# Kernel tuning notes

Hardware: AMD Instinct MI355X
Metric: run time of the kernel (lower is better)

The kernel has to match this reference:

```python
import jax, jax.numpy as jnp
import numpy as np
import math

H = 8
C = 512
HIDE = 2048
LN_EPS = 1e-6


def setup_inputs() -> dict:
    key = jax.random.key(0)
    ks = jax.random.split(key, 9)
    B, N = 4, 2048
    std = 0.02
    return {
        "q": jax.random.normal(ks[0], (B, N, C), jnp.float32),
        "k": jax.random.normal(ks[1], (B, N, C), jnp.float32),
        "v": jax.random.normal(ks[2], (B, N, C), jnp.float32),
        "fc1_w": jax.random.normal(ks[3], (HIDE, C), jnp.float32) * std,
        "fc1_b": jnp.zeros((HIDE,), jnp.float32),
        "fc2_w": jax.random.normal(ks[4], (C, HIDE), jnp.float32) * std,
        "fc2_b": jnp.zeros((C,), jnp.float32),
        "ln1_w": jnp.ones((C,), jnp.float32),
        "ln1_b": jnp.zeros((C,), jnp.float32),
        "ln2_w": jnp.ones((C,), jnp.float32),
        "ln2_b": jnp.zeros((C,), jnp.float32),
    }


def _layernorm(x, w, b):
    mu = jnp.mean(x, axis=-1, keepdims=True)
    var = jnp.var(x, axis=-1, keepdims=True)
    return (x - mu) * jax.lax.rsqrt(var + LN_EPS) * w + b


def _mha(q, k, v):
    B, N, _ = q.shape
    hd = C // H
    # [B, H, N, hd]
    qh = q.reshape(B, N, H, hd).transpose(0, 2, 1, 3)
    kh = k.reshape(B, N, H, hd).transpose(0, 2, 1, 3)
    vh = v.reshape(B, N, H, hd).transpose(0, 2, 1, 3)
    scores = jnp.einsum('bhqd,bhkd->bhqk', qh, kh) / math.sqrt(hd)
    probs = jax.nn.softmax(scores, axis=-1)
    out = jnp.einsum('bhqk,bhkd->bhqd', probs, vh)
    return out.transpose(0, 2, 1, 3).reshape(B, N, C)


def reference(q, k, v, fc1_w, fc1_b, fc2_w, fc2_b, ln1_w, ln1_b, ln2_w, ln2_b):
    attn = _mha(q, k, v)
    q2 = _layernorm(q + attn, ln1_w, ln1_b)
    h = jax.nn.gelu(q2 @ fc1_w.T + fc1_b, approximate=False)
    mlp = h @ fc2_w.T + fc2_b
    return _layernorm(q2 + mlp, ln2_w, ln2_b)
```

## Files before the change

kernel.cpp:

```cpp
#include <hip/hip_runtime.h>
#include <math.h>

typedef unsigned short u16;
typedef __bf16 bf16_t;
typedef bf16_t bf16x4 __attribute__((ext_vector_type(4)));
typedef bf16_t bf16x8 __attribute__((ext_vector_type(8)));
typedef short s16x4 __attribute__((ext_vector_type(4)));
typedef float f32x4 __attribute__((ext_vector_type(4)));

typedef const __attribute__((address_space(1))) void* gcp;
typedef __attribute__((address_space(3))) void* lcp;

#define BB 4
#define NN 2048
#define CC 512
#define HH 8
#define HD 64
#define HIDE_ 2048
#define TT (BB*NN)

#if __has_builtin(__builtin_amdgcn_exp2f)
#define EXP2(x) __builtin_amdgcn_exp2f(x)
#else
#define EXP2(x) __expf((x) * 0.69314718055994531f)
#endif

#if __has_builtin(__builtin_amdgcn_rcpf)
#define RCP(x) __builtin_amdgcn_rcpf(x)
#else
#define RCP(x) (1.0f / (x))
#endif

__device__ __forceinline__ u16 f2bf(float f) {
  unsigned u = __float_as_uint(f);
  u += 0x7FFF + ((u >> 16) & 1);
  return (u16)(u >> 16);
}

__device__ __forceinline__ void bf8_to_f(const u16* p, float* f) {
  uint4 u = *(const uint4*)p;
  f[0] = __uint_as_float(u.x << 16); f[1] = __uint_as_float(u.x & 0xffff0000u);
  f[2] = __uint_as_float(u.y << 16); f[3] = __uint_as_float(u.y & 0xffff0000u);
  f[4] = __uint_as_float(u.z << 16); f[5] = __uint_as_float(u.z & 0xffff0000u);
  f[6] = __uint_as_float(u.w << 16); f[7] = __uint_as_float(u.w & 0xffff0000u);
}

__device__ __forceinline__ float gelu_tanh(float x) {
  float y = 0.7978845608028654f * x * (1.0f + 0.044715f * x * x);
  float a = y * 2.8853900817779268f;
  a = fminf(fmaxf(a, -30.0f), 30.0f);
  float e = EXP2(a);
  float t = (e - 1.0f) * RCP(e + 1.0f);
  return 0.5f * x * (1.0f + t);
}

__global__ __launch_bounds__(256) void prep_kernel(const float* __restrict__ q,
                                                   const float* __restrict__ k,
                                                   const float* __restrict__ fc1w,
                                                   const float* __restrict__ fc2w,
                                                   const float* __restrict__ v,
                                                   u16* __restrict__ qb,
                                                   u16* __restrict__ kb,
                                                   u16* __restrict__ w1b,
                                                   u16* __restrict__ w2b,
                                                   u16* __restrict__ vtb,
                                                   float qscale) {
  __shared__ __align__(16) u16 T[64 * 72];
  int bid = blockIdx.x, tid = threadIdx.x;
  if (bid < 5120) {
    const float* in;
    u16* out;
    int rel;
    float sc = 1.0f;
    if (bid < 2048)      { in = q;    out = qb;  rel = bid;        sc = qscale; }
    else if (bid < 4096) { in = k;    out = kb;  rel = bid - 2048; }
    else if (bid < 4608) { in = fc1w; out = w1b; rel = bid - 4096; }
    else                 { in = fc2w; out = w2b; rel = bid - 4608; }
    int i = (rel * 256 + tid) * 8;
    float4 a = *(const float4*)(in + i);
    float4 b2 = *(const float4*)(in + i + 4);
    u16 r[8] = {f2bf(a.x * sc), f2bf(a.y * sc), f2bf(a.z * sc), f2bf(a.w * sc),
                f2bf(b2.x * sc), f2bf(b2.y * sc), f2bf(b2.z * sc), f2bf(b2.w * sc)};
    *(uint4*)(out + i) = *(const uint4*)r;
    return;
  }
  int tv = bid - 5120;
  int j0 = (tv & 31) * 64;
  int bh = tv >> 5;
  int b = bh >> 3, h = bh & 7;
#pragma unroll
  for (int i = 0; i < 16; i++) {
    int idx = i * 256 + tid;
    int j = idx >> 6, d = idx & 63;
    T[d * 72 + j] = f2bf(v[((size_t)(b * NN + j0 + j)) * CC + h * 64 + d]);
  }
  __syncthreads();
#pragma unroll
  for (int i = 0; i < 16; i++) {
    int idx = i * 256 + tid;
    int d = idx >> 6, j = idx & 63;
    vtb[((size_t)(bh * 64 + d)) * NN + j0 + j] = T[d * 72 + j];
  }
}

__global__ __launch_bounds__(256, 8) void attn_kernel(const u16* __restrict__ qb,
                                                      const u16* __restrict__ kb,
                                                      const u16* __restrict__ vtb,
                                                      float* __restrict__ ou,
                                                      float* __restrict__ lsum) {
  __shared__ __align__(16) u16 Ks[64 * 64];
  __shared__ __align__(16) u16 Vs[64 * 64];
  int tid = threadIdx.x, wave = tid >> 6, lane = tid & 63;
  int l15 = lane & 15, quad = lane >> 4;
  int r7 = l15 & 7;
  int bid = blockIdx.x;
  int half = blockIdx.y;
  int qt = bid & 31, h = (bid >> 5) & 7, b = bid >> 8;
  int qw = qt * 64 + wave * 16;
  int j0base = half * 1024;

  float* ou_ = ou + (size_t)half * TT * CC;
  float* ls_ = lsum + (size_t)half * TT * HH;

  size_t qbase = ((size_t)(b * NN + qw + l15)) * CC + h * 64 + quad * 8;
  bf16x8 qf0 = *(const bf16x8*)&qb[qbase];
  bf16x8 qf1 = *(const bf16x8*)&qb[qbase + 32];

  int rl = lane >> 3;
  int cb = (lane & 7) ^ rl;
  int rK = wave * 16 + rl;
  size_t vtbase = ((size_t)(b * HH + h)) * 64 * NN;
  const u16* kp0 = kb + ((size_t)(b * NN + j0base + rK)) * CC + h * 64 + cb * 8;
  const u16* kp1 = kp0 + (size_t)8 * CC;
  const u16* vp0 = vtb + vtbase + (size_t)rK * NN + j0base + cb * 8;
  const u16* vp1 = vp0 + (size_t)8 * NN;
  lcp lK0 = (lcp)&Ks[wave * 16 * 64];
  lcp lK1 = (lcp)&Ks[wave * 16 * 64 + 8 * 64];
  lcp lV0 = (lcp)&Vs[wave * 16 * 64];
  lcp lV1 = (lcp)&Vs[wave * 16 * 64 + 8 * 64];

  float l_p = 0.f;
  f32x4 o[4] = {};

  for (int kt = 0; kt < 16; kt++) {
    __syncthreads();
    __builtin_amdgcn_global_load_lds((gcp)kp0, lK0, 16, 0, 0);
    __builtin_amdgcn_global_load_lds((gcp)kp1, lK1, 16, 0, 0);
    __builtin_amdgcn_global_load_lds((gcp)vp0, lV0, 16, 0, 0);
    __builtin_amdgcn_global_load_lds((gcp)vp1, lV1, 16, 0, 0);
    kp0 += (size_t)64 * CC; kp1 += (size_t)64 * CC;
    vp0 += 64; vp1 += 64;
    __syncthreads();

    s16x4 pf[4];
#pragma unroll
    for (int nt = 0; nt < 4; nt++) {
      f32x4 z = {0.f, 0.f, 0.f, 0.f};
      const u16* krow = &Ks[(nt * 16 + l15) * 64];
      bf16x8 k0 = *(const bf16x8*)&krow[(quad ^ r7) * 8];
      bf16x8 k1 = *(const bf16x8*)&krow[((quad + 4) ^ r7) * 8];
      z = __builtin_amdgcn_mfma_f32_16x16x32_bf16(k0, qf0, z, 0, 0, 0);
      z = __builtin_amdgcn_mfma_f32_16x16x32_bf16(k1, qf1, z, 0, 0, 0);
      float p0 = EXP2(z[0]), p1 = EXP2(z[1]);
      float p2 = EXP2(z[2]), p3 = EXP2(z[3]);
      l_p += (p0 + p1) + (p2 + p3);
      bf16x4 tv = {(bf16_t)p0, (bf16_t)p1, (bf16_t)p2, (bf16_t)p3};
      pf[nt] = __builtin_bit_cast(s16x4, tv);
    }
#pragma unroll
    for (int dt = 0; dt < 4; dt++) {
      const u16* vrow = &Vs[(dt * 16 + l15) * 64];
#pragma unroll
      for (int nt = 0; nt < 4; nt++) {
        s16x4 vf = *(const s16x4*)
            &vrow[((nt * 2 + (quad >> 1)) ^ r7) * 8 + (quad & 1) * 4];
        o[dt] = __builtin_amdgcn_mfma_f32_16x16x16bf16_1k(vf, pf[nt], o[dt], 0, 0, 0);
      }
    }
  }

  l_p += __shfl_xor(l_p, 16, 64);
  l_p += __shfl_xor(l_p, 32, 64);
  if (quad == 0) ls_[(size_t)(b * NN + qw + l15) * HH + h] = l_p;
  size_t obase = ((size_t)(b * NN + qw + l15)) * CC + h * 64 + quad * 4;
#pragma unroll
  for (int dt = 0; dt < 4; dt++)
    *(f32x4*)&ou_[obase + dt * 16] = o[dt];
}

__global__ __launch_bounds__(256) void ln1_kernel(const float* __restrict__ q,
                                                  const float* __restrict__ ou,
                                                  const float* __restrict__ lsum,
                                                  const float* __restrict__ w,
                                                  const float* __restrict__ bb,
                                                  u16* __restrict__ outb) {
  int tid = threadIdx.x;
  int row = blockIdx.x * 4 + (tid >> 6);
  int lane = tid & 63;
  int h = lane >> 3;
  size_t base = (size_t)row * CC + lane * 8;
  const float* ou1 = ou + (size_t)TT * CC;
  const float* ls1 = lsum + (size_t)TT * HH;
  float li = lsum[(size_t)row * HH + h] + ls1[(size_t)row * HH + h];
  float inv = 1.0f / li;
  float4 a0 = *(const float4*)(q + base);
  float4 a1 = *(const float4*)(q + base + 4);
  float4 c0 = *(const float4*)(ou + base);
  float4 c1 = *(const float4*)(ou + base + 4);
  float4 d0 = *(const float4*)(ou1 + base);
  float4 d1 = *(const float4*)(ou1 + base + 4);
  float x[8] = {a0.x + (c0.x + d0.x) * inv, a0.y + (c0.y + d0.y) * inv,
                a0.z + (c0.z + d0.z) * inv, a0.w + (c0.w + d0.w) * inv,
                a1.x + (c1.x + d1.x) * inv, a1.y + (c1.y + d1.y) * inv,
                a1.z + (c1.z + d1.z) * inv, a1.w + (c1.w + d1.w) * inv};
  float sum = 0.f, sq = 0.f;
#pragma unroll
  for (int i = 0; i < 8; i++) { sum += x[i]; sq += x[i] * x[i]; }
#pragma unroll
  for (int msk = 1; msk < 64; msk <<= 1) {
    sum += __shfl_xor(sum, msk, 64);
    sq += __shfl_xor(sq, msk, 64);
  }
  float mu = sum * (1.0f / CC);
  float var = sq * (1.0f / CC) - mu * mu;
  float rs = rsqrtf(var + 1e-6f);
  int col = lane * 8;
  float4 w0 = *(const float4*)(w + col);
  float4 w1 = *(const float4*)(w + col + 4);
  float4 b0 = *(const float4*)(bb + col);
  float4 b1 = *(const float4*)(bb + col + 4);
  float wv[8] = {w0.x, w0.y, w0.z, w0.w, w1.x, w1.y, w1.z, w1.w};
  float bv[8] = {b0.x, b0.y, b0.z, b0.w, b1.x, b1.y, b1.z, b1.w};
  u16 r[8];
#pragma unroll
  for (int i = 0; i < 8; i++) r[i] = f2bf((x[i] - mu) * rs * wv[i] + bv[i]);
  *(uint4*)(outb + base) = *(const uint4*)r;
}

__global__ __launch_bounds__(256) void ln2_kernel(const u16* __restrict__ q2b,
                                                  const u16* __restrict__ mp,
                                                  const float* __restrict__ fb,
                                                  const float* __restrict__ w,
                                                  const float* __restrict__ bb,
                                                  float* __restrict__ outf) {
  int tid = threadIdx.x;
  int row = blockIdx.x * 4 + (tid >> 6);
  int lane = tid & 63;
  size_t base = (size_t)row * CC + lane * 8;
  const u16* mp1 = mp + (size_t)TT * CC;
  int col = lane * 8;
  float a[8], c[8], d[8];
  bf8_to_f(q2b + base, a);
  bf8_to_f(mp + base, c);
  bf8_to_f(mp1 + base, d);
  float4 f0 = *(const float4*)(fb + col);
  float4 f1 = *(const float4*)(fb + col + 4);
  float fbv[8] = {f0.x, f0.y, f0.z, f0.w, f1.x, f1.y, f1.z, f1.w};
  float x[8];
#pragma unroll
  for (int i = 0; i < 8; i++) x[i] = a[i] + c[i] + d[i] + fbv[i];
  float sum = 0.f, sq = 0.f;
#pragma unroll
  for (int i = 0; i < 8; i++) { sum += x[i]; sq += x[i] * x[i]; }
#pragma unroll
  for (int msk = 1; msk < 64; msk <<= 1) {
    sum += __shfl_xor(sum, msk, 64);
    sq += __shfl_xor(sq, msk, 64);
  }
  float mu = sum * (1.0f / CC);
  float var = sq * (1.0f / CC) - mu * mu;
  float rs = rsqrtf(var + 1e-6f);
  float4 w0 = *(const float4*)(w + col);
  float4 w1 = *(const float4*)(w + col + 4);
  float4 b0 = *(const float4*)(bb + col);
  float4 b1 = *(const float4*)(bb + col + 4);
  float wv[8] = {w0.x, w0.y, w0.z, w0.w, w1.x, w1.y, w1.z, w1.w};
  float bv[8] = {b0.x, b0.y, b0.z, b0.w, b1.x, b1.y, b1.z, b1.w};
  float y[8];
#pragma unroll
  for (int i = 0; i < 8; i++) y[i] = (x[i] - mu) * rs * wv[i] + bv[i];
  *(float4*)(outf + base) = make_float4(y[0], y[1], y[2], y[3]);
  *(float4*)(outf + base + 4) = make_float4(y[4], y[5], y[6], y[7]);
}

__global__ __launch_bounds__(256) void gemm_fc1(const u16* __restrict__ A,
                                                const u16* __restrict__ Bw,
                                                const float* __restrict__ bias,
                                                u16* __restrict__ outb,
                                                int M, int Nn, int K) {
  __shared__ __align__(16) u16 As[128 * 32];
  __shared__ __align__(16) u16 Bs[128 * 32];
  int tid = threadIdx.x, wave = tid >> 6, lane = tid & 63;
  int l15 = lane & 15, quad = lane >> 4;
  int m0 = blockIdx.y * 128, n0 = blockIdx.x * 128;
  int wm = (wave >> 1) * 64, wn = (wave & 1) * 64;
  int w32 = wave * 32;
  int lrow = lane >> 2, lcol = (lane & 3) * 8;
  const u16* Ap = &A[(size_t)(m0 + w32 + lrow) * K + lcol];
  const u16* Bp = &Bw[(size_t)(n0 + w32 + lrow) * K + lcol];
  const u16* Ap2 = Ap + (size_t)16 * K;
  const u16* Bp2 = Bp + (size_t)16 * K;
  lcp lAs0 = (lcp)&As[w32 * 32];
  lcp lAs1 = (lcp)&As[(w32 + 16) * 32];
  lcp lBs0 = (lcp)&Bs[w32 * 32];
  lcp lBs1 = (lcp)&Bs[(w32 + 16) * 32];
  f32x4 acc[4][4] = {};

  for (int kk = 0; kk < K; kk += 32) {
    __syncthreads();
    __builtin_amdgcn_global_load_lds((gcp)(Ap + kk), lAs0, 16, 0, 0);
    __builtin_amdgcn_global_load_lds((gcp)(Ap2 + kk), lAs1, 16, 0, 0);
    __builtin_amdgcn_global_load_lds((gcp)(Bp + kk), lBs0, 16, 0, 0);
    __builtin_amdgcn_global_load_lds((gcp)(Bp2 + kk), lBs1, 16, 0, 0);
    __syncthreads();
    bf16x8 af[4], bf[4];
#pragma unroll
    for (int am = 0; am < 4; am++)
      af[am] = *(const bf16x8*)&As[(wm + am * 16 + l15) * 32 + quad * 8];
#pragma unroll
    for (int bn = 0; bn < 4; bn++)
      bf[bn] = *(const bf16x8*)&Bs[(wn + bn * 16 + l15) * 32 + quad * 8];
#pragma unroll
    for (int am = 0; am < 4; am++)
#pragma unroll
      for (int bn = 0; bn < 4; bn++)
        acc[am][bn] =
            __builtin_amdgcn_mfma_f32_16x16x32_bf16(af[am], bf[bn], acc[am][bn], 0, 0, 0);
  }

#pragma unroll
  for (int am = 0; am < 4; am++)
#pragma unroll
    for (int bn = 0; bn < 4; bn++) {
      int rowi = m0 + wm + am * 16 + quad * 4;
      int col = n0 + wn + bn * 16 + l15;
      float bcol = bias[col];
#pragma unroll
      for (int r = 0; r < 4; r++) {
        float val = gelu_tanh(acc[am][bn][r] + bcol);
        outb[(size_t)(rowi + r) * Nn + col] = f2bf(val);
      }
    }
}

__global__ __launch_bounds__(256) void gemm_fc2_sk(const u16* __restrict__ A,
                                                   const u16* __restrict__ Bw,
                                                   u16* __restrict__ outb,
                                                   int M, int Nn, int K, int Ksplit) {
  __shared__ __align__(16) u16 As[128 * 32];
  __shared__ __align__(16) u16 Bs[64 * 32];
  int tid = threadIdx.x, wave = tid >> 6, lane = tid & 63;
  int l15 = lane & 15, quad = lane >> 4;
  int m0 = blockIdx.y * 128, n0 = blockIdx.x * 64;
  int kbeg = blockIdx.z * Ksplit;
  u16* outz = outb + (size_t)blockIdx.z * TT * CC;
  int wm = wave * 32;
  int lrow = lane >> 2, lcol = (lane & 3) * 8;
  const u16* Ap = &A[(size_t)(m0 + wm + lrow) * K + lcol];
  const u16* Ap2 = Ap + (size_t)16 * K;
  const u16* Bp = &Bw[(size_t)(n0 + wave * 16 + lrow) * K + lcol];
  lcp lAs0 = (lcp)&As[wm * 32];
  lcp lAs1 = (lcp)&As[(wm + 16) * 32];
  lcp lBs = (lcp)&Bs[wave * 16 * 32];
  f32x4 acc[2][4] = {};

  for (int kk = kbeg; kk < kbeg + Ksplit; kk += 32) {
    __syncthreads();
    __builtin_amdgcn_global_load_lds((gcp)(Ap + kk), lAs0, 16, 0, 0);
    __builtin_amdgcn_global_load_lds((gcp)(Ap2 + kk), lAs1, 16, 0, 0);
    __builtin_amdgcn_global_load_lds((gcp)(Bp + kk), lBs, 16, 0, 0);
    __syncthreads();
    bf16x8 af[2], bf[4];
#pragma unroll
    for (int am = 0; am < 2; am++)
      af[am] = *(const bf16x8*)&As[(wm + am * 16 + l15) * 32 + quad * 8];
#pragma unroll
    for (int bn = 0; bn < 4; bn++)
      bf[bn] = *(const bf16x8*)&Bs[(bn * 16 + l15) * 32 + quad * 8];
#pragma unroll
    for (int am = 0; am < 2; am++)
#pragma unroll
      for (int bn = 0; bn < 4; bn++)
        acc[am][bn] =
            __builtin_amdgcn_mfma_f32_16x16x32_bf16(af[am], bf[bn], acc[am][bn], 0, 0, 0);
  }

#pragma unroll
  for (int am = 0; am < 2; am++)
#pragma unroll
    for (int bn = 0; bn < 4; bn++) {
      int rowi = m0 + wm + am * 16 + quad * 4;
      int col = n0 + bn * 16 + l15;
#pragma unroll
      for (int r = 0; r < 4; r++)
        outz[(size_t)(rowi + r) * Nn + col] = f2bf(acc[am][bn][r]);
    }
}

extern "C" void kernel_launch(void* const* d_in, const int* in_sizes, int n_in,
                              void* d_out, int out_size, void* d_ws, size_t ws_size,
                              hipStream_t stream) {
  const float* q = (const float*)d_in[0];
  const float* k = (const float*)d_in[1];
  const float* v = (const float*)d_in[2];
  const float* fc1_w = (const float*)d_in[3];
  const float* fc1_b = (const float*)d_in[4];
  const float* fc2_w = (const float*)d_in[5];
  const float* fc2_b = (const float*)d_in[6];
  const float* ln1_w = (const float*)d_in[7];
  const float* ln1_b = (const float*)d_in[8];
  const float* ln2_w = (const float*)d_in[9];
  const float* ln2_b = (const float*)d_in[10];
  float* out = (float*)d_out;

  char* ws = (char*)d_ws;
  size_t off = 0;
  u16* qb = (u16*)(ws + off); off += (size_t)TT * CC * 2;
  u16* kb = (u16*)(ws + off); off += (size_t)TT * CC * 2;
  u16* vtb = (u16*)(ws + off); off += (size_t)TT * CC * 2;
  u16* w1b = (u16*)(ws + off); off += (size_t)HIDE_ * CC * 2;
  u16* w2b = (u16*)(ws + off); off += (size_t)CC * HIDE_ * 2;
  float* ou = (float*)(ws + off); off += (size_t)2 * TT * CC * 4;
  u16* hbuf = (u16*)ou;
  float* lsum = (float*)(ws + off); off += (size_t)2 * TT * HH * 4;
  u16* q2b = (u16*)(ws + off); off += (size_t)TT * CC * 2;
  u16* mp = (u16*)(ws + off); off += (size_t)2 * TT * CC * 2;

  prep_kernel<<<6144, 256, 0, stream>>>(q, k, fc1_w, fc2_w, v, qb, kb, w1b, w2b, vtb,
                                        0.18033688011112042f);
  attn_kernel<<<dim3(1024, 2), 256, 0, stream>>>(qb, kb, vtb, ou, lsum);
  ln1_kernel<<<2048, 256, 0, stream>>>(q, ou, lsum, ln1_w, ln1_b, q2b);
  gemm_fc1<<<dim3(16, 64), 256, 0, stream>>>(q2b, w1b, fc1_b, hbuf, TT, HIDE_, CC);
  gemm_fc2_sk<<<dim3(8, 64, 2), 256, 0, stream>>>(hbuf, w2b, mp, TT, CC, HIDE_, 1024);
  ln2_kernel<<<2048, 256, 0, stream>>>(q2b, mp, fc2_b, ln2_w, ln2_b, out);
}
```

Baseline: 259.9 us.

## Double attention query tile per wave, store bf16 intermediates, widen fc2 tile

```diff
diff --git a/kernel.cpp b/kernel.cpp
--- a/kernel.cpp
+++ b/kernel.cpp
@@ -103,10 +103,10 @@
   }
 }
 
-__global__ __launch_bounds__(256, 8) void attn_kernel(const u16* __restrict__ qb,
+__global__ __launch_bounds__(256, 4) void attn_kernel(const u16* __restrict__ qb,
                                                       const u16* __restrict__ kb,
                                                       const u16* __restrict__ vtb,
-                                                      float* __restrict__ ou,
+                                                      u16* __restrict__ ou,
                                                       float* __restrict__ lsum) {
   __shared__ __align__(16) u16 Ks[64 * 64];
   __shared__ __align__(16) u16 Vs[64 * 64];
@@ -115,16 +115,18 @@
   int r7 = l15 & 7;
   int bid = blockIdx.x;
   int half = blockIdx.y;
-  int qt = bid & 31, h = (bid >> 5) & 7, b = bid >> 8;
-  int qw = qt * 64 + wave * 16;
+  int qt = bid & 15, h = (bid >> 4) & 7, b = bid >> 7;
+  int qw = qt * 128 + wave * 32;
   int j0base = half * 1024;
 
-  float* ou_ = ou + (size_t)half * TT * CC;
+  u16* ou_ = ou + (size_t)half * TT * CC;
   float* ls_ = lsum + (size_t)half * TT * HH;
 
   size_t qbase = ((size_t)(b * NN + qw + l15)) * CC + h * 64 + quad * 8;
-  bf16x8 qf0 = *(const bf16x8*)&qb[qbase];
-  bf16x8 qf1 = *(const bf16x8*)&qb[qbase + 32];
+  bf16x8 qfA0 = *(const bf16x8*)&qb[qbase];
+  bf16x8 qfA1 = *(const bf16x8*)&qb[qbase + 32];
+  bf16x8 qfB0 = *(const bf16x8*)&qb[qbase + (size_t)16 * CC];
+  bf16x8 qfB1 = *(const bf16x8*)&qb[qbase + (size_t)16 * CC + 32];
 
   int rl = lane >> 3;
   int cb = (lane & 7) ^ rl;
@@ -139,8 +141,8 @@
   lcp lV0 = (lcp)&Vs[wave * 16 * 64];
   lcp lV1 = (lcp)&Vs[wave * 16 * 64 + 8 * 64];
 
-  float l_p = 0.f;
-  f32x4 o[4] = {};
+  float lA = 0.f, lB = 0.f;
+  f32x4 oA[4] = {}, oB[4] = {};
 
   for (int kt = 0; kt < 16; kt++) {
     __syncthreads();
@@ -152,20 +154,25 @@
     vp0 += 64; vp1 += 64;
     __syncthreads();
 
-    s16x4 pf[4];
+    s16x4 pfA[4], pfB[4];
 #pragma unroll
     for (int nt = 0; nt < 4; nt++) {
-      f32x4 z = {0.f, 0.f, 0.f, 0.f};
       const u16* krow = &Ks[(nt * 16 + l15) * 64];
       bf16x8 k0 = *(const bf16x8*)&krow[(quad ^ r7) * 8];
       bf16x8 k1 = *(const bf16x8*)&krow[((quad + 4) ^ r7) * 8];
-      z = __builtin_amdgcn_mfma_f32_16x16x32_bf16(k0, qf0, z, 0, 0, 0);
-      z = __builtin_amdgcn_mfma_f32_16x16x32_bf16(k1, qf1, z, 0, 0, 0);
-      float p0 = EXP2(z[0]), p1 = EXP2(z[1]);
-      float p2 = EXP2(z[2]), p3 = EXP2(z[3]);
-      l_p += (p0 + p1) + (p2 + p3);
-      bf16x4 tv = {(bf16_t)p0, (bf16_t)p1, (bf16_t)p2, (bf16_t)p3};
-      pf[nt] = __builtin_bit_cast(s16x4, tv);
+      f32x4 zA = {0.f, 0.f, 0.f, 0.f}, zB = {0.f, 0.f, 0.f, 0.f};
+      zA = __builtin_amdgcn_mfma_f32_16x16x32_bf16(k0, qfA0, zA, 0, 0, 0);
+      zA = __builtin_amdgcn_mfma_f32_16x16x32_bf16(k1, qfA1, zA, 0, 0, 0);
+      zB = __builtin_amdgcn_mfma_f32_16x16x32_bf16(k0, qfB0, zB, 0, 0, 0);
+      zB = __builtin_amdgcn_mfma_f32_16x16x32_bf16(k1, qfB1, zB, 0, 0, 0);
+      float a0 = EXP2(zA[0]), a1 = EXP2(zA[1]), a2 = EXP2(zA[2]), a3 = EXP2(zA[3]);
+      float b0 = EXP2(zB[0]), b1 = EXP2(zB[1]), b2 = EXP2(zB[2]), b3 = EXP2(zB[3]);
+      lA += (a0 + a1) + (a2 + a3);
+      lB += (b0 + b1) + (b2 + b3);
+      bf16x4 ta = {(bf16_t)a0, (bf16_t)a1, (bf16_t)a2, (bf16_t)a3};
+      bf16x4 tb = {(bf16_t)b0, (bf16_t)b1, (bf16_t)b2, (bf16_t)b3};
+      pfA[nt] = __builtin_bit_cast(s16x4, ta);
+      pfB[nt] = __builtin_bit_cast(s16x4, tb);
     }
 #pragma unroll
     for (int dt = 0; dt < 4; dt++) {
@@ -174,45 +181,53 @@
       for (int nt = 0; nt < 4; nt++) {
         s16x4 vf = *(const s16x4*)
             &vrow[((nt * 2 + (quad >> 1)) ^ r7) * 8 + (quad & 1) * 4];
-        o[dt] = __builtin_amdgcn_mfma_f32_16x16x16bf16_1k(vf, pf[nt], o[dt], 0, 0, 0);
+        oA[dt] = __builtin_amdgcn_mfma_f32_16x16x16bf16_1k(vf, pfA[nt], oA[dt], 0, 0, 0);
+        oB[dt] = __builtin_amdgcn_mfma_f32_16x16x16bf16_1k(vf, pfB[nt], oB[dt], 0, 0, 0);
       }
     }
   }
 
-  l_p += __shfl_xor(l_p, 16, 64);
-  l_p += __shfl_xor(l_p, 32, 64);
-  if (quad == 0) ls_[(size_t)(b * NN + qw + l15) * HH + h] = l_p;
+  lA += __shfl_xor(lA, 16, 64);
+  lA += __shfl_xor(lA, 32, 64);
+  lB += __shfl_xor(lB, 16, 64);
+  lB += __shfl_xor(lB, 32, 64);
+  if (quad == 0) {
+    ls_[(size_t)(b * NN + qw + l15) * HH + h] = lA;
+    ls_[(size_t)(b * NN + qw + 16 + l15) * HH + h] = lB;
+  }
   size_t obase = ((size_t)(b * NN + qw + l15)) * CC + h * 64 + quad * 4;
 #pragma unroll
-  for (int dt = 0; dt < 4; dt++)
-    *(f32x4*)&ou_[obase + dt * 16] = o[dt];
-}
-
-__global__ __launch_bounds__(256) void ln1_kernel(const float* __restrict__ q,
-                                                  const float* __restrict__ ou,
+  for (int dt = 0; dt < 4; dt++) {
+    u16 ra[4] = {f2bf(oA[dt][0]), f2bf(oA[dt][1]), f2bf(oA[dt][2]), f2bf(oA[dt][3])};
+    u16 rb[4] = {f2bf(oB[dt][0]), f2bf(oB[dt][1]), f2bf(oB[dt][2]), f2bf(oB[dt][3])};
+    *(uint2*)&ou_[obase + dt * 16] = *(const uint2*)ra;
+    *(uint2*)&ou_[obase + (size_t)16 * CC + dt * 16] = *(const uint2*)rb;
+  }
+}
+
+__global__ __launch_bounds__(256) void ln1_kernel(const u16* __restrict__ qb,
+                                                  const u16* __restrict__ ou,
                                                   const float* __restrict__ lsum,
                                                   const float* __restrict__ w,
                                                   const float* __restrict__ bb,
-                                                  u16* __restrict__ outb) {
+                                                  u16* __restrict__ outb,
+                                                  float inv_qs) {
   int tid = threadIdx.x;
   int row = blockIdx.x * 4 + (tid >> 6);
   int lane = tid & 63;
   int h = lane >> 3;
   size_t base = (size_t)row * CC + lane * 8;
-  const float* ou1 = ou + (size_t)TT * CC;
+  const u16* ou1 = ou + (size_t)TT * CC;
   const float* ls1 = lsum + (size_t)TT * HH;
   float li = lsum[(size_t)row * HH + h] + ls1[(size_t)row * HH + h];
   float inv = 1.0f / li;
-  float4 a0 = *(const float4*)(q + base);
-  float4 a1 = *(const float4*)(q + base + 4);
-  float4 c0 = *(const float4*)(ou + base);
-  float4 c1 = *(const float4*)(ou + base + 4);
-  float4 d0 = *(const float4*)(ou1 + base);
-  float4 d1 = *(const float4*)(ou1 + base + 4);
-  float x[8] = {a0.x + (c0.x + d0.x) * inv, a0.y + (c0.y + d0.y) * inv,
-                a0.z + (c0.z + d0.z) * inv, a0.w + (c0.w + d0.w) * inv,
-                a1.x + (c1.x + d1.x) * inv, a1.y + (c1.y + d1.y) * inv,
-                a1.z + (c1.z + d1.z) * inv, a1.w + (c1.w + d1.w) * inv};
+  float a[8], c[8], d[8];
+  bf8_to_f(qb + base, a);
+  bf8_to_f(ou + base, c);
+  bf8_to_f(ou1 + base, d);
+  float x[8];
+#pragma unroll
+  for (int i = 0; i < 8; i++) x[i] = a[i] * inv_qs + (c[i] + d[i]) * inv;
   float sum = 0.f, sq = 0.f;
 #pragma unroll
   for (int i = 0; i < 8; i++) { sum += x[i]; sq += x[i] * x[i]; }
@@ -348,37 +363,41 @@
                                                    u16* __restrict__ outb,
                                                    int M, int Nn, int K, int Ksplit) {
   __shared__ __align__(16) u16 As[128 * 32];
-  __shared__ __align__(16) u16 Bs[64 * 32];
+  __shared__ __align__(16) u16 Bs[128 * 32];
   int tid = threadIdx.x, wave = tid >> 6, lane = tid & 63;
   int l15 = lane & 15, quad = lane >> 4;
-  int m0 = blockIdx.y * 128, n0 = blockIdx.x * 64;
+  int m0 = blockIdx.y * 128, n0 = blockIdx.x * 128;
   int kbeg = blockIdx.z * Ksplit;
   u16* outz = outb + (size_t)blockIdx.z * TT * CC;
-  int wm = wave * 32;
+  int wm = (wave >> 1) * 64, wn = (wave & 1) * 64;
+  int w32 = wave * 32;
   int lrow = lane >> 2, lcol = (lane & 3) * 8;
-  const u16* Ap = &A[(size_t)(m0 + wm + lrow) * K + lcol];
+  const u16* Ap = &A[(size_t)(m0 + w32 + lrow) * K + lcol];
+  const u16* Bp = &Bw[(size_t)(n0 + w32 + lrow) * K + lcol];
   const u16* Ap2 = Ap + (size_t)16 * K;
-  const u16* Bp = &Bw[(size_t)(n0 + wave * 16 + lrow) * K + lcol];
-  lcp lAs0 = (lcp)&As[wm * 32];
-  lcp lAs1 = (lcp)&As[(wm + 16) * 32];
-  lcp lBs = (lcp)&Bs[wave * 16 * 32];
-  f32x4 acc[2][4] = {};
+  const u16* Bp2 = Bp + (size_t)16 * K;
+  lcp lAs0 = (lcp)&As[w32 * 32];
+  lcp lAs1 = (lcp)&As[(w32 + 16) * 32];
+  lcp lBs0 = (lcp)&Bs[w32 * 32];
+  lcp lBs1 = (lcp)&Bs[(w32 + 16) * 32];
+  f32x4 acc[4][4] = {};
 
   for (int kk = kbeg; kk < kbeg + Ksplit; kk += 32) {
     __syncthreads();
     __builtin_amdgcn_global_load_lds((gcp)(Ap + kk), lAs0, 16, 0, 0);
     __builtin_amdgcn_global_load_lds((gcp)(Ap2 + kk), lAs1, 16, 0, 0);
-    __builtin_amdgcn_global_load_lds((gcp)(Bp + kk), lBs, 16, 0, 0);
-    __syncthreads();
-    bf16x8 af[2], bf[4];
-#pragma unroll
-    for (int am = 0; am < 2; am++)
+    __builtin_amdgcn_global_load_lds((gcp)(Bp + kk), lBs0, 16, 0, 0);
+    __builtin_amdgcn_global_load_lds((gcp)(Bp2 + kk), lBs1, 16, 0, 0);
+    __syncthreads();
+    bf16x8 af[4], bf[4];
+#pragma unroll
+    for (int am = 0; am < 4; am++)
       af[am] = *(const bf16x8*)&As[(wm + am * 16 + l15) * 32 + quad * 8];
 #pragma unroll
     for (int bn = 0; bn < 4; bn++)
-      bf[bn] = *(const bf16x8*)&Bs[(bn * 16 + l15) * 32 + quad * 8];
-#pragma unroll
-    for (int am = 0; am < 2; am++)
+      bf[bn] = *(const bf16x8*)&Bs[(wn + bn * 16 + l15) * 32 + quad * 8];
+#pragma unroll
+    for (int am = 0; am < 4; am++)
 #pragma unroll
       for (int bn = 0; bn < 4; bn++)
         acc[am][bn] =
@@ -386,11 +405,11 @@
   }
 
 #pragma unroll
-  for (int am = 0; am < 2; am++)
+  for (int am = 0; am < 4; am++)
 #pragma unroll
     for (int bn = 0; bn < 4; bn++) {
       int rowi = m0 + wm + am * 16 + quad * 4;
-      int col = n0 + bn * 16 + l15;
+      int col = n0 + wn + bn * 16 + l15;
 #pragma unroll
       for (int r = 0; r < 4; r++)
         outz[(size_t)(rowi + r) * Nn + col] = f2bf(acc[am][bn][r]);
@@ -420,17 +439,18 @@
   u16* vtb = (u16*)(ws + off); off += (size_t)TT * CC * 2;
   u16* w1b = (u16*)(ws + off); off += (size_t)HIDE_ * CC * 2;
   u16* w2b = (u16*)(ws + off); off += (size_t)CC * HIDE_ * 2;
-  float* ou = (float*)(ws + off); off += (size_t)2 * TT * CC * 4;
-  u16* hbuf = (u16*)ou;
+  u16* ou = (u16*)(ws + off); off += (size_t)2 * TT * CC * 2;
   float* lsum = (float*)(ws + off); off += (size_t)2 * TT * HH * 4;
   u16* q2b = (u16*)(ws + off); off += (size_t)TT * CC * 2;
+  u16* hbuf = (u16*)(ws + off); off += (size_t)TT * HIDE_ * 2;
   u16* mp = (u16*)(ws + off); off += (size_t)2 * TT * CC * 2;
 
-  prep_kernel<<<6144, 256, 0, stream>>>(q, k, fc1_w, fc2_w, v, qb, kb, w1b, w2b, vtb,
-                                        0.18033688011112042f);
-  attn_kernel<<<dim3(1024, 2), 256, 0, stream>>>(qb, kb, vtb, ou, lsum);
-  ln1_kernel<<<2048, 256, 0, stream>>>(q, ou, lsum, ln1_w, ln1_b, q2b);
+  const float QS = 0.18033688011112042f;
+  const float INV_QS = 5.5451774444795623f;
+  prep_kernel<<<6144, 256, 0, stream>>>(q, k, fc1_w, fc2_w, v, qb, kb, w1b, w2b, vtb, QS);
+  attn_kernel<<<dim3(512, 2), 256, 0, stream>>>(qb, kb, vtb, ou, lsum);
+  ln1_kernel<<<2048, 256, 0, stream>>>(qb, ou, lsum, ln1_w, ln1_b, q2b, INV_QS);
   gemm_fc1<<<dim3(16, 64), 256, 0, stream>>>(q2b, w1b, fc1_b, hbuf, TT, HIDE_, CC);
-  gemm_fc2_sk<<<dim3(8, 64, 2), 256, 0, stream>>>(hbuf, w2b, mp, TT, CC, HIDE_, 1024);
+  gemm_fc2_sk<<<dim3(4, 64, 2), 256, 0, stream>>>(hbuf, w2b, mp, TT, CC, HIDE_, 1024);
   ln2_kernel<<<2048, 256, 0, stream>>>(q2b, mp, fc2_b, ln2_w, ln2_b, out);
 }
```

After: 242.3 us. -6.8%, faster.
